# Performance work log

Hardware: AMD Instinct MI355X
Metric: run time of the kernel (lower is better)

The kernel has to match this reference:

```python
import math
import jax, jax.numpy as jnp
import numpy as np

N_HEAD = 16
N_EMBD = 1024
HEAD_DIM = N_EMBD // N_HEAD  # 64
GROUP_SIZE = 64
RESIDUAL_LEN = 32
K_BITS = 2
V_BITS = 2
CLIP = 10000.0


def _fake_quant(x, mn, mx, bits):
    # asymmetric min-max quantize-dequantize with straight-through estimator
    qmax = float(2 ** bits - 1)
    scale = jnp.maximum((mx - mn) / qmax, 1e-8)
    q = jnp.round((x - mn) / scale)
    deq = q * scale + mn
    return x + jax.lax.stop_gradient(deq - x)


def quantize_key(k):
    # per-channel over token groups: [B,H,S,D] -> groups of GROUP_SIZE tokens,
    # min/max over the token axis within each group, per head_dim channel
    B, H, S, D = k.shape
    k = jnp.clip(k, -CLIP, CLIP)
    kg = k.reshape(B, H, S // GROUP_SIZE, GROUP_SIZE, D)
    mn = kg.min(axis=3, keepdims=True)
    mx = kg.max(axis=3, keepdims=True)
    return _fake_quant(kg, mn, mx, K_BITS).reshape(B, H, S, D)


def quantize_value(v):
    # per-token over channel groups: groups of GROUP_SIZE along head_dim
    B, H, S, D = v.shape
    g = GROUP_SIZE if (GROUP_SIZE > 0 and D % GROUP_SIZE == 0) else D
    v = jnp.clip(v, -CLIP, CLIP)
    vg = v.reshape(B, H, S, D // g, g)
    mn = vg.min(axis=-1, keepdims=True)
    mx = vg.max(axis=-1, keepdims=True)
    return _fake_quant(vg, mn, mx, V_BITS).reshape(B, H, S, D)


def setup_inputs() -> dict:
    key = jax.random.key(0)
    ks = jax.random.split(key, 5)
    B, S = 2, 2048
    scale_in = 1.0 / math.sqrt(N_EMBD)
    return {
        "x": jax.random.normal(ks[0], (B, S, N_EMBD), jnp.float32),
        "W_qkv": jax.random.normal(ks[1], (N_EMBD, 3 * N_EMBD), jnp.float32) * scale_in,
        "b_qkv": jax.random.normal(ks[2], (3 * N_EMBD,), jnp.float32) * 0.01,
        "W_proj": jax.random.normal(ks[3], (N_EMBD, N_EMBD), jnp.float32) * scale_in,
        "b_proj": jax.random.normal(ks[4], (N_EMBD,), jnp.float32) * 0.01,
    }


def reference(x, W_qkv, b_qkv, W_proj, b_proj):
    B, S, E = x.shape
    H, D = N_HEAD, HEAD_DIM
    qkv = x @ W_qkv + b_qkv                       # [B,S,3E]
    q, k, v = jnp.split(qkv, 3, axis=-1)
    split = lambda t: t.reshape(B, S, H, D).transpose(0, 2, 1, 3)  # [B,H,S,D]
    q, k, v = split(q), split(k), split(v)

    # KIVI: quantize all keys up to multiple of RESIDUAL_LEN, values except last RESIDUAL_LEN tokens
    if S > RESIDUAL_LEN:
        kql = (S // RESIDUAL_LEN) * RESIDUAL_LEN
        if kql > 0:
            k = jnp.concatenate([quantize_key(k[:, :, :kql]), k[:, :, kql:]], axis=2)
        vql = max(0, S - RESIDUAL_LEN)
        if vql > 0:
            v = jnp.concatenate([quantize_value(v[:, :, :vql]), v[:, :, vql:]], axis=2)

    attn = jnp.einsum("bhqd,bhkd->bhqk", q, k) / math.sqrt(D)
    if S > 1:
        mask = jnp.tril(jnp.ones((S, S), bool))
        attn = jnp.where(mask[None, None], attn, -jnp.inf)
    att = jax.nn.softmax(attn, axis=-1)
    y = jnp.einsum("bhqk,bhkd->bhqd", att, v)     # [B,H,S,D]
    y = y.transpose(0, 2, 1, 3).reshape(B, S, E)
    return y @ W_proj + b_proj
```

## Files before the change

kernel.cpp:

```cpp
#include <hip/hip_runtime.h>
#include <math.h>

#define BATCH 2
#define SEQ   2048
#define NHEAD 16
#define EMB   1024
#define N3E   3072
#define VQL   2016
#define REC_CAP 65536

typedef unsigned short ushort8_t __attribute__((ext_vector_type(8)));
typedef unsigned short ushort4_t __attribute__((ext_vector_type(4)));
typedef short bf16x8 __attribute__((ext_vector_type(8)));
typedef float f32x4 __attribute__((ext_vector_type(4)));
typedef unsigned int uint2_t __attribute__((ext_vector_type(2)));

struct __align__(16) Rec { unsigned dst; unsigned mn_pack; float mn; float scale; };

__device__ __forceinline__ float clipf(float x) {
    return fminf(fmaxf(x, -10000.0f), 10000.0f);
}
__device__ __forceinline__ float bf2f(unsigned short u) {
    return __uint_as_float(((unsigned)u) << 16);
}
__device__ __forceinline__ unsigned short f2bf(float f) {
    unsigned u = __float_as_uint(f);
    unsigned r = 0x7FFFu + ((u >> 16) & 1u);
    return (unsigned short)((u + r) >> 16);
}
__device__ __forceinline__ unsigned cvtpk(float lo, float hi) {
    unsigned r;
    asm("v_cvt_pk_bf16_f32 %0, %1, %2" : "=v"(r) : "v"(lo), "v"(hi));
    return r;
}
__device__ __forceinline__ void async_copy16(const unsigned short* g, unsigned short* lds) {
    __builtin_amdgcn_global_load_lds(
        (const __attribute__((address_space(1))) unsigned int*)g,
        (__attribute__((address_space(3))) unsigned int*)lds, 16, 0, 0);
}

__global__ __launch_bounds__(256) void split_x_kernel(
    const float* __restrict__ X,
    unsigned short* __restrict__ Xh, unsigned short* __restrict__ Xm,
    unsigned* __restrict__ cnt)
{
    if (blockIdx.x == 0 && threadIdx.x == 0) *cnt = 0;
    const size_t i8 = ((size_t)blockIdx.x * 256 + threadIdx.x) * 8;
    float4 a = *(const float4*)(X + i8);
    float4 b = *(const float4*)(X + i8 + 4);
    float xs[8] = {a.x, a.y, a.z, a.w, b.x, b.y, b.z, b.w};
    ushort8_t h8, m8;
    #pragma unroll
    for (int j = 0; j < 8; ++j) {
        unsigned short h = f2bf(xs[j]);
        h8[j] = h;
        m8[j] = f2bf(xs[j] - bf2f(h));
    }
    *(ushort8_t*)(Xh + i8) = h8;
    *(ushort8_t*)(Xm + i8) = m8;
}

__global__ __launch_bounds__(256) void split_wt_kernel(
    const float* __restrict__ W,
    unsigned short* __restrict__ WTh, unsigned short* __restrict__ WTm,
    unsigned short* __restrict__ WTl)
{
    __shared__ float t[64][65];
    const int tid = threadIdx.x;
    const int nt = blockIdx.x * 64, kt = blockIdx.y * 64;
    const int r = tid >> 2, cg = (tid & 3) * 16;
    #pragma unroll
    for (int j = 0; j < 4; ++j) {
        float4 v = *(const float4*)(W + (size_t)(kt + r) * N3E + nt + cg + j * 4);
        t[r][cg + j * 4 + 0] = v.x; t[r][cg + j * 4 + 1] = v.y;
        t[r][cg + j * 4 + 2] = v.z; t[r][cg + j * 4 + 3] = v.w;
    }
    __syncthreads();
    ushort8_t h8[2], m8[2], l8[2];
    #pragma unroll
    for (int j = 0; j < 16; ++j) {
        float v = t[cg + j][r];
        unsigned short h = f2bf(v);
        float r1 = v - bf2f(h);
        unsigned short mm = f2bf(r1);
        float r2 = r1 - bf2f(mm);
        h8[j >> 3][j & 7] = h; m8[j >> 3][j & 7] = mm; l8[j >> 3][j & 7] = f2bf(r2);
    }
    size_t off = (size_t)(nt + r) * 1024 + kt + cg;
    *(ushort8_t*)(WTh + off) = h8[0]; *(ushort8_t*)(WTh + off + 8) = h8[1];
    *(ushort8_t*)(WTm + off) = m8[0]; *(ushort8_t*)(WTm + off + 8) = m8[1];
    *(ushort8_t*)(WTl + off) = l8[0]; *(ushort8_t*)(WTl + off + 8) = l8[1];
}

__device__ __forceinline__ void push_flag(unsigned* cnt, Rec* recs, unsigned dst,
                                          int mg, int ng, float mn, float scale) {
    unsigned idx = atomicAdd(cnt, 1u);
    if (idx < REC_CAP) {
        Rec r; r.dst = dst; r.mn_pack = (unsigned)mg | ((unsigned)ng << 12);
        r.mn = mn; r.scale = scale;
        recs[idx] = r;
    }
}

__global__ __launch_bounds__(256, 2) void gemm_qkv3(
    const unsigned short* __restrict__ Xh, const unsigned short* __restrict__ Xm,
    const unsigned short* __restrict__ WTh, const unsigned short* __restrict__ WTm,
    const float* __restrict__ bias,
    unsigned short* __restrict__ Qb, unsigned short* __restrict__ Kb,
    unsigned short* __restrict__ Vt,
    unsigned* __restrict__ cnt, Rec* __restrict__ recs)
{
    __shared__ __align__(16) unsigned short LDS[2][4][128 * 32];

    const int tid  = threadIdx.x;
    const int wave = tid >> 6, lane = tid & 63, lr = lane & 15, g = lane >> 4;
    const int wr = wave >> 1, wc = wave & 1;
    const int row0 = blockIdx.y * 128, col0 = blockIdx.x * 128;

    const int drow = lane >> 2;
    const int sgr  = ((lane & 3) ^ ((lane >> 3) & 3)) * 8;
    const unsigned short* tsrc =
        (wave == 0) ? Xh  + (size_t)(row0 + drow) * 1024 + sgr :
        (wave == 1) ? Xm  + (size_t)(row0 + drow) * 1024 + sgr :
        (wave == 2) ? WTh + (size_t)(col0 + drow) * 1024 + sgr :
                      WTm + (size_t)(col0 + drow) * 1024 + sgr;

    #define STAGE(buf, t)                                                        \
        _Pragma("unroll")                                                        \
        for (int c = 0; c < 8; ++c)                                              \
            async_copy16(tsrc + (size_t)(c * 16) * 1024 + (t) * 32,              \
                         &LDS[buf][wave][c * 16 * 32]);

    f32x4 acc[4][4] = {};

    const int rgr = (g ^ ((lr >> 1) & 3)) * 8;

    STAGE(0, 0);
    STAGE(1, 1);

    for (int t = 0; t < 32; ++t) {
        const int cur = t & 1;
        if (t < 31) {
            asm volatile("s_waitcnt vmcnt(8)" ::: "memory");
        } else {
            asm volatile("s_waitcnt vmcnt(0)" ::: "memory");
        }
        __builtin_amdgcn_s_barrier();

        bf16x8 axh[4], axm[4], bwh[4], bwm[4];
        #pragma unroll
        for (int mf = 0; mf < 4; ++mf) {
            axh[mf] = *(const bf16x8*)&LDS[cur][0][(wr * 64 + mf * 16 + lr) * 32 + rgr];
            axm[mf] = *(const bf16x8*)&LDS[cur][1][(wr * 64 + mf * 16 + lr) * 32 + rgr];
        }
        #pragma unroll
        for (int nf = 0; nf < 4; ++nf) {
            bwh[nf] = *(const bf16x8*)&LDS[cur][2][(wc * 64 + nf * 16 + lr) * 32 + rgr];
            bwm[nf] = *(const bf16x8*)&LDS[cur][3][(wc * 64 + nf * 16 + lr) * 32 + rgr];
        }
        asm volatile("s_waitcnt lgkmcnt(0)" ::: "memory");
        __builtin_amdgcn_sched_barrier(0);
        __builtin_amdgcn_s_barrier();

        if (t < 30) { STAGE(cur, t + 2); }

        #pragma unroll
        for (int nf = 0; nf < 4; ++nf) {
            #pragma unroll
            for (int mf = 0; mf < 4; ++mf)
                acc[mf][nf] = __builtin_amdgcn_mfma_f32_16x16x32_bf16(
                    axh[mf], bwh[nf], acc[mf][nf], 0, 0, 0);
            #pragma unroll
            for (int mf = 0; mf < 4; ++mf)
                acc[mf][nf] = __builtin_amdgcn_mfma_f32_16x16x32_bf16(
                    axh[mf], bwm[nf], acc[mf][nf], 0, 0, 0);
            #pragma unroll
            for (int mf = 0; mf < 4; ++mf)
                acc[mf][nf] = __builtin_amdgcn_mfma_f32_16x16x32_bf16(
                    axm[mf], bwh[nf], acc[mf][nf], 0, 0, 0);
        }
    }
    #undef STAGE

    const int which = col0 >> 10;
    const int hcol  = ((col0 + wc * 64) & 1023) >> 6;
    const int b     = row0 >> 11;
    const int s_base = (row0 & 2047) + wr * 64;

    float bo[4];
    #pragma unroll
    for (int n = 0; n < 4; ++n) bo[n] = bias[col0 + wc * 64 + n * 16 + lr];
    #pragma unroll
    for (int m = 0; m < 4; ++m)
        #pragma unroll
        for (int n = 0; n < 4; ++n)
            #pragma unroll
            for (int r = 0; r < 4; ++r)
                acc[m][n][r] += bo[n];

    if (which == 0) {
        unsigned short* qdst = Qb + (((size_t)b * NHEAD + hcol) * SEQ) * 64;
        #pragma unroll
        for (int m = 0; m < 4; ++m)
            #pragma unroll
            for (int r = 0; r < 4; ++r) {
                int s = s_base + m * 16 + g * 4 + r;
                #pragma unroll
                for (int n = 0; n < 4; ++n)
                    qdst[(size_t)s * 64 + n * 16 + lr] = f2bf(acc[m][n][r]);
            }
    } else if (which == 1) {
        #pragma unroll
        for (int n = 0; n < 4; ++n) {
            float cmn = INFINITY, cmx = -INFINITY;
            #pragma unroll
            for (int m = 0; m < 4; ++m)
                #pragma unroll
                for (int r = 0; r < 4; ++r) {
                    float v = clipf(acc[m][n][r]);
                    acc[m][n][r] = v;
                    cmn = fminf(cmn, v); cmx = fmaxf(cmx, v);
                }
            cmn = fminf(cmn, __shfl_xor(cmn, 16)); cmx = fmaxf(cmx, __shfl_xor(cmx, 16));
            cmn = fminf(cmn, __shfl_xor(cmn, 32)); cmx = fmaxf(cmx, __shfl_xor(cmx, 32));
            float scale = fmaxf((cmx - cmn) / 3.0f, 1e-8f);
            float tol = 0.5f - 1e-3f / scale;
            #pragma unroll
            for (int m = 0; m < 4; ++m)
                #pragma unroll
                for (int r = 0; r < 4; ++r) {
                    float f = (acc[m][n][r] - cmn) / scale;
                    float qv = rintf(f);
                    if (fabsf(f - qv) > tol) {
                        int s  = s_base + m * 16 + g * 4 + r;
                        int mg = row0 + wr * 64 + m * 16 + g * 4 + r;
                        int ng = col0 + wc * 64 + n * 16 + lr;
                        unsigned dst = 4194304u +
                            (unsigned)(((b * NHEAD + hcol) * SEQ + s) * 64 + n * 16 + lr);
                        push_flag(cnt, recs, dst, mg, ng, cmn, scale);
                    }
                    acc[m][n][r] = qv * scale + cmn;
                }
        }
        unsigned short* kdst = Kb + (((size_t)b * NHEAD + hcol) * SEQ) * 64;
        #pragma unroll
        for (int m = 0; m < 4; ++m)
            #pragma unroll
            for (int r = 0; r < 4; ++r) {
                int s = s_base + m * 16 + g * 4 + r;
                #pragma unroll
                for (int n = 0; n < 4; ++n)
                    kdst[(size_t)s * 64 + n * 16 + lr] = f2bf(acc[m][n][r]);
            }
    } else {
        #pragma unroll
        for (int m = 0; m < 4; ++m)
            #pragma unroll
            for (int r = 0; r < 4; ++r) {
                float c[4];
                #pragma unroll
                for (int n = 0; n < 4; ++n) c[n] = clipf(acc[m][n][r]);
                float mn = fminf(fminf(c[0], c[1]), fminf(c[2], c[3]));
                float mx = fmaxf(fmaxf(c[0], c[1]), fmaxf(c[2], c[3]));
                #pragma unroll
                for (int msk = 1; msk < 16; msk <<= 1) {
                    mn = fminf(mn, __shfl_xor(mn, msk));
                    mx = fmaxf(mx, __shfl_xor(mx, msk));
                }
                int s = s_base + m * 16 + g * 4 + r;
                if (s < VQL) {
                    float scale = fmaxf((mx - mn) / 3.0f, 1e-8f);
                    float tol = 0.5f - 1e-3f / scale;
                    #pragma unroll
                    for (int n = 0; n < 4; ++n) {
                        float f = (c[n] - mn) / scale;
                        float qv = rintf(f);
                        if (fabsf(f - qv) > tol) {
                            int mg = row0 + wr * 64 + m * 16 + g * 4 + r;
                            int ng = col0 + wc * 64 + n * 16 + lr;
                            unsigned dst = 8388608u +
                                (unsigned)((((b * NHEAD + hcol) * 64) + n * 16 + lr) * SEQ + s);
                            push_flag(cnt, recs, dst, mg, ng, mn, scale);
                        }
                        acc[m][n][r] = qv * scale + mn;
                    }
                }
            }
        #pragma unroll
        for (int m = 0; m < 4; ++m)
            #pragma unroll
            for (int n = 0; n < 4; ++n) {
                ushort4_t o;
                #pragma unroll
                for (int r = 0; r < 4; ++r) o[r] = f2bf(acc[m][n][r]);
                *(ushort4_t*)(Vt + ((((size_t)b * NHEAD + hcol) * 64) + n * 16 + lr) * SEQ
                                 + s_base + m * 16 + g * 4) = o;
            }
    }
}

__global__ __launch_bounds__(256) void repair_kernel(
    const float* __restrict__ X,
    const unsigned short* __restrict__ WTh, const unsigned short* __restrict__ WTm,
    const unsigned short* __restrict__ WTl,
    const float* __restrict__ bias, unsigned short* __restrict__ wsu,
    const unsigned* __restrict__ cnt, const Rec* __restrict__ recs)
{
    const int lane = threadIdx.x & 63;
    const int wid  = blockIdx.x * 4 + (threadIdx.x >> 6);
    unsigned nrec = *cnt; if (nrec > REC_CAP) nrec = REC_CAP;
    for (unsigned i = wid; i < nrec; i += gridDim.x * 4) {
        Rec rc = recs[i];
        int mg = rc.mn_pack & 4095;
        int ng = (rc.mn_pack >> 12) & 4095;
        const float* xr          = X   + (size_t)mg * 1024 + lane * 16;
        const unsigned short* wh = WTh + (size_t)ng * 1024 + lane * 16;
        const unsigned short* wm = WTm + (size_t)ng * 1024 + lane * 16;
        const unsigned short* wl = WTl + (size_t)ng * 1024 + lane * 16;
        float s = 0.f;
        #pragma unroll
        for (int j4 = 0; j4 < 4; ++j4) {
            float4 xv = *(const float4*)(xr + j4 * 4);
            float xs[4] = {xv.x, xv.y, xv.z, xv.w};
            #pragma unroll
            for (int e = 0; e < 4; ++e) {
                int j = j4 * 4 + e;
                s += xs[e] * (bf2f(wh[j]) + bf2f(wm[j]) + bf2f(wl[j]));
            }
        }
        #pragma unroll
        for (int msk = 1; msk < 64; msk <<= 1) s += __shfl_xor(s, msk);
        if (lane == 0) {
            float v = clipf(s + bias[ng]);
            float val = rintf((v - rc.mn) / rc.scale) * rc.scale + rc.mn;
            wsu[rc.dst] = f2bf(val);
        }
    }
}

__global__ __launch_bounds__(256) void attn_mfma(
    unsigned short* __restrict__ QY,
    const unsigned short* __restrict__ K,
    const unsigned short* __restrict__ Vt)
{
    __shared__ unsigned short Ks [64][72];
    __shared__ unsigned short VsT[64][72];
    __shared__ unsigned short Ps [4][16][72];

    const int tid  = threadIdx.x;
    const int wave = tid >> 6;
    const int lane = tid & 63;
    const int lr   = lane & 15;
    const int g    = lane >> 4;

    const int bid = blockIdx.x;
    const int qt  = 31 - (bid >> 5);
    const int bh  = bid & 31;
    const size_t base = (size_t)bh * (SEQ * 64);

    const int qrow = qt * 64 + wave * 16 + lr;
    const unsigned short* qp = QY + base + (size_t)qrow * 64;
    bf16x8 aq[2];
    #pragma unroll
    for (int ka = 0; ka < 2; ++ka)
        aq[ka] = *(const bf16x8*)(qp + ka * 32 + g * 8);

    f32x4 o[4] = {};
    float m[4]    = {-1e30f, -1e30f, -1e30f, -1e30f};
    float lsum[4] = {};
    const float sc = 0.125f;

    const int str = tid >> 2;
    const int stc = (tid & 3) << 4;

    for (int jt = 0; jt <= qt; ++jt) {
        __syncthreads();
        {
            const unsigned short* kg = K + base + ((size_t)(jt * 64 + str) << 6) + stc;
            *(ushort8_t*)&Ks[str][stc]     = *(const ushort8_t*)kg;
            *(ushort8_t*)&Ks[str][stc + 8] = *(const ushort8_t*)(kg + 8);
            const unsigned short* vg = Vt + base + ((size_t)str << 11) + jt * 64 + stc;
            *(ushort8_t*)&VsT[str][stc]     = *(const ushort8_t*)vg;
            *(ushort8_t*)&VsT[str][stc + 8] = *(const ushort8_t*)(vg + 8);
        }
        __syncthreads();

        f32x4 s[4] = {};
        #pragma unroll
        for (int f = 0; f < 4; ++f) {
            #pragma unroll
            for (int ka = 0; ka < 2; ++ka) {
                bf16x8 bk = *(const bf16x8*)&Ks[f * 16 + lr][ka * 32 + g * 8];
                s[f] = __builtin_amdgcn_mfma_f32_16x16x32_bf16(aq[ka], bk, s[f], 0, 0, 0);
            }
        }

        const bool diag = (jt == qt);
        float mx[4];
        #pragma unroll
        for (int r = 0; r < 4; ++r) {
            const int ql = wave * 16 + g * 4 + r;
            float vmax = -1e30f;
            #pragma unroll
            for (int f = 0; f < 4; ++f) {
                float v = s[f][r] * sc;
                if (diag && (f * 16 + lr) > ql) v = -1e30f;
                s[f][r] = v;
                vmax = fmaxf(vmax, v);
            }
            mx[r] = vmax;
        }
        #pragma unroll
        for (int msk = 1; msk < 16; msk <<= 1)
            #pragma unroll
            for (int r = 0; r < 4; ++r)
                mx[r] = fmaxf(mx[r], __shfl_xor(mx[r], msk));

        float alpha[4], tsum[4];
        #pragma unroll
        for (int r = 0; r < 4; ++r) {
            float mn = fmaxf(m[r], mx[r]);
            alpha[r] = __expf(m[r] - mn);
            m[r] = mn;
            float ts = 0.0f;
            #pragma unroll
            for (int f = 0; f < 4; ++f) {
                float p = __expf(s[f][r] - mn);
                unsigned short ub = f2bf(p);
                Ps[wave][g * 4 + r][f * 16 + lr] = ub;
                ts += bf2f(ub);
            }
            tsum[r] = ts;
        }
        #pragma unroll
        for (int msk = 1; msk < 16; msk <<= 1)
            #pragma unroll
            for (int r = 0; r < 4; ++r)
                tsum[r] += __shfl_xor(tsum[r], msk);
        #pragma unroll
        for (int r = 0; r < 4; ++r) {
            lsum[r] = lsum[r] * alpha[r] + tsum[r];
            #pragma unroll
            for (int df = 0; df < 4; ++df) o[df][r] *= alpha[r];
        }

        asm volatile("s_waitcnt lgkmcnt(0)" ::: "memory");
        __builtin_amdgcn_sched_barrier(0);

        bf16x8 pa[2];
        #pragma unroll
        for (int kb = 0; kb < 2; ++kb)
            pa[kb] = *(const bf16x8*)&Ps[wave][lr][kb * 32 + g * 8];
        #pragma unroll
        for (int df = 0; df < 4; ++df) {
            #pragma unroll
            for (int kb = 0; kb < 2; ++kb) {
                bf16x8 vb = *(const bf16x8*)&VsT[df * 16 + lr][kb * 32 + g * 8];
                o[df] = __builtin_amdgcn_mfma_f32_16x16x32_bf16(pa[kb], vb, o[df], 0, 0, 0);
            }
        }
    }

    float invl[4];
    #pragma unroll
    for (int r = 0; r < 4; ++r) invl[r] = 1.0f / lsum[r];
    #pragma unroll
    for (int df = 0; df < 4; ++df)
        #pragma unroll
        for (int r = 0; r < 4; ++r) {
            int q = qt * 64 + wave * 16 + g * 4 + r;
            QY[base + (size_t)q * 64 + df * 16 + lr] = f2bf(o[df][r] * invl[r]);
        }
}

#define PJ_PAD 72
__global__ __launch_bounds__(256, 2) void gemm_proj_mfma(
    const unsigned short* __restrict__ Y, const float* __restrict__ W,
    const float* __restrict__ bias, float* __restrict__ C)
{
    __shared__ unsigned short A2[2][128][PJ_PAD];
    __shared__ unsigned short B2[2][128][PJ_PAD];

    const int tid  = threadIdx.x;
    const int wave = tid >> 6, lane = tid & 63, lr = lane & 15, g = lane >> 4;
    const int wr = wave >> 1, wc = wave & 1;
    const int row0 = blockIdx.y * 128, col0 = blockIdx.x * 128;
    const int b = row0 >> 11, s0 = row0 & 2047;

    const int ra  = tid >> 1,       ca  = (tid & 1) * 32;
    const int cb4 = (tid & 31) * 4, kb4 = (tid >> 5) * 4;

    ushort8_t a_reg[4];
    float bw[2][4][4];

    {
        const unsigned short* gy = Y + ((((size_t)b * NHEAD + 0) * SEQ + s0 + ra) << 6) + ca;
        #pragma unroll
        for (int i = 0; i < 4; ++i) a_reg[i] = *(const ushort8_t*)(gy + i * 8);
        const float* gw = W + (size_t)kb4 * EMB + col0 + cb4;
        #pragma unroll
        for (int half = 0; half < 2; ++half)
            #pragma unroll
            for (int i = 0; i < 4; ++i)
                *(float4*)bw[half][i] = *(const float4*)(gw + (size_t)(half * 32 + i) * EMB);
        #pragma unroll
        for (int i = 0; i < 4; ++i) *(ushort8_t*)&A2[0][ra][ca + i * 8] = a_reg[i];
        #pragma unroll
        for (int half = 0; half < 2; ++half)
            #pragma unroll
            for (int j = 0; j < 4; ++j) {
                unsigned w2[2];
                w2[0] = cvtpk(bw[half][0][j], bw[half][1][j]);
                w2[1] = cvtpk(bw[half][2][j], bw[half][3][j]);
                *(uint2_t*)&B2[0][cb4 + j][half * 32 + kb4] = *(uint2_t*)w2;
            }
    }
    __syncthreads();

    f32x4 acc[4][4] = {};

    for (int t = 0; t < 16; ++t) {
        const int cur = t & 1;
        if (t < 15) {
            const unsigned short* gy =
                Y + ((((size_t)b * NHEAD + (t + 1)) * SEQ + s0 + ra) << 6) + ca;
            #pragma unroll
            for (int i = 0; i < 4; ++i) a_reg[i] = *(const ushort8_t*)(gy + i * 8);
            const float* gw = W + (size_t)((t + 1) * 64 + kb4) * EMB + col0 + cb4;
            #pragma unroll
            for (int half = 0; half < 2; ++half)
                #pragma unroll
                for (int i = 0; i < 4; ++i)
                    *(float4*)bw[half][i] = *(const float4*)(gw + (size_t)(half * 32 + i) * EMB);
        }
        #pragma unroll
        for (int kk = 0; kk < 2; ++kk) {
            bf16x8 af[4];
            #pragma unroll
            for (int m = 0; m < 4; ++m)
                af[m] = *(const bf16x8*)&A2[cur][wr * 64 + m * 16 + lr][kk * 32 + g * 8];
            #pragma unroll
            for (int n = 0; n < 4; ++n) {
                bf16x8 bf = *(const bf16x8*)&B2[cur][wc * 64 + n * 16 + lr][kk * 32 + g * 8];
                #pragma unroll
                for (int m = 0; m < 4; ++m)
                    acc[m][n] = __builtin_amdgcn_mfma_f32_16x16x32_bf16(af[m], bf, acc[m][n], 0, 0, 0);
            }
        }
        if (t < 15) {
            const int nxt = cur ^ 1;
            #pragma unroll
            for (int i = 0; i < 4; ++i) *(ushort8_t*)&A2[nxt][ra][ca + i * 8] = a_reg[i];
            #pragma unroll
            for (int half = 0; half < 2; ++half)
                #pragma unroll
                for (int j = 0; j < 4; ++j) {
                    unsigned w2[2];
                    w2[0] = cvtpk(bw[half][0][j], bw[half][1][j]);
                    w2[1] = cvtpk(bw[half][2][j], bw[half][3][j]);
                    *(uint2_t*)&B2[nxt][cb4 + j][half * 32 + kb4] = *(uint2_t*)w2;
                }
        }
        __syncthreads();
    }

    float bo[4];
    #pragma unroll
    for (int n = 0; n < 4; ++n) bo[n] = bias[col0 + wc * 64 + n * 16 + lr];
    #pragma unroll
    for (int m = 0; m < 4; ++m)
        #pragma unroll
        for (int r = 0; r < 4; ++r) {
            int mrow = row0 + wr * 64 + m * 16 + g * 4 + r;
            #pragma unroll
            for (int n = 0; n < 4; ++n)
                C[(size_t)mrow * EMB + col0 + wc * 64 + n * 16 + lr] = acc[m][n][r] + bo[n];
        }
}

extern "C" void kernel_launch(void* const* d_in, const int* in_sizes, int n_in,
                              void* d_out, int out_size, void* d_ws, size_t ws_size,
                              hipStream_t stream)
{
    const float* x     = (const float*)d_in[0];
    const float* Wqkv  = (const float*)d_in[1];
    const float* bqkv  = (const float*)d_in[2];
    const float* Wproj = (const float*)d_in[3];
    const float* bproj = (const float*)d_in[4];
    float* out = (float*)d_out;

    char* ws = (char*)d_ws;
    unsigned short* q   = (unsigned short*)ws;
    unsigned short* kb  = (unsigned short*)(ws + (8u  << 20));
    unsigned short* vt  = (unsigned short*)(ws + (16u << 20));
    unsigned short* Xh  = (unsigned short*)(ws + (24u << 20));
    unsigned short* Xm  = (unsigned short*)(ws + (32u << 20));
    unsigned short* WTh = (unsigned short*)(ws + (40u << 20));
    unsigned short* WTm = (unsigned short*)(ws + (46u << 20));
    unsigned short* WTl = (unsigned short*)(ws + (52u << 20));
    unsigned*       cnt = (unsigned*)(ws + (58u << 20));
    Rec*           recs = (Rec*)(ws + (58u << 20) + 256);

    split_x_kernel<<<2048, 256, 0, stream>>>(x, Xh, Xm, cnt);
    split_wt_kernel<<<dim3(48, 16), 256, 0, stream>>>(Wqkv, WTh, WTm, WTl);
    gemm_qkv3<<<dim3(N3E / 128, 4096 / 128), 256, 0, stream>>>(
        Xh, Xm, WTh, WTm, bqkv, q, kb, vt, cnt, recs);
    repair_kernel<<<128, 256, 0, stream>>>(x, WTh, WTm, WTl, bqkv,
                                           (unsigned short*)d_ws, cnt, recs);
    attn_mfma<<<dim3(32 * 32), 256, 0, stream>>>(q, kb, vt);
    gemm_proj_mfma<<<dim3(EMB / 128, 4096 / 128), 256, 0, stream>>>(q, Wproj, bproj, out);
}
```

Measured before the change: 321.9 us.

## Interleave LDS B-fragment loads with MFMA clusters in QKV GEMM loop

Splits the QKV GEMM inner loop so the B-fragment LDS reads for later column fragments are issued while MFMAs for earlier fragments run, with partial lgkmcnt waits instead of one full wait. Three of the four MFMA clusters run before the second barrier and the stage refill, and the last runs after the next async copy has been issued. s_setprio raises wave priority around the MFMA clusters. This is meant to hide LDS latency and overlap global prefetch with compute, but it depends on the manual wait counts being correct and may raise register pressure.

```diff
diff --git a/kernel.cpp b/kernel.cpp
--- a/kernel.cpp
+++ b/kernel.cpp
@@ -131,9 +131,25 @@
             async_copy16(tsrc + (size_t)(c * 16) * 1024 + (t) * 32,              \
                          &LDS[buf][wave][c * 16 * 32]);
 
+    #define CLUSTER(BH, BM, NF)                                                  \
+        _Pragma("unroll")                                                        \
+        for (int mf = 0; mf < 4; ++mf)                                           \
+            acc[mf][NF] = __builtin_amdgcn_mfma_f32_16x16x32_bf16(               \
+                axh[mf], BH, acc[mf][NF], 0, 0, 0);                              \
+        _Pragma("unroll")                                                        \
+        for (int mf = 0; mf < 4; ++mf)                                           \
+            acc[mf][NF] = __builtin_amdgcn_mfma_f32_16x16x32_bf16(               \
+                axh[mf], BM, acc[mf][NF], 0, 0, 0);                              \
+        _Pragma("unroll")                                                        \
+        for (int mf = 0; mf < 4; ++mf)                                           \
+            acc[mf][NF] = __builtin_amdgcn_mfma_f32_16x16x32_bf16(               \
+                axm[mf], BH, acc[mf][NF], 0, 0, 0);
+
     f32x4 acc[4][4] = {};
 
     const int rgr = (g ^ ((lr >> 1) & 3)) * 8;
+    const int arow = wr * 64 + lr;
+    const int brow = wc * 64 + lr;
 
     STAGE(0, 0);
     STAGE(1, 1);
@@ -147,40 +163,51 @@
         }
         __builtin_amdgcn_s_barrier();
 
-        bf16x8 axh[4], axm[4], bwh[4], bwm[4];
+        bf16x8 axh[4], axm[4];
         #pragma unroll
         for (int mf = 0; mf < 4; ++mf) {
-            axh[mf] = *(const bf16x8*)&LDS[cur][0][(wr * 64 + mf * 16 + lr) * 32 + rgr];
-            axm[mf] = *(const bf16x8*)&LDS[cur][1][(wr * 64 + mf * 16 + lr) * 32 + rgr];
-        }
-        #pragma unroll
-        for (int nf = 0; nf < 4; ++nf) {
-            bwh[nf] = *(const bf16x8*)&LDS[cur][2][(wc * 64 + nf * 16 + lr) * 32 + rgr];
-            bwm[nf] = *(const bf16x8*)&LDS[cur][3][(wc * 64 + nf * 16 + lr) * 32 + rgr];
-        }
+            axh[mf] = *(const bf16x8*)&LDS[cur][0][(arow + mf * 16) * 32 + rgr];
+            axm[mf] = *(const bf16x8*)&LDS[cur][1][(arow + mf * 16) * 32 + rgr];
+        }
+        bf16x8 bh0 = *(const bf16x8*)&LDS[cur][2][(brow +  0) * 32 + rgr];
+        bf16x8 bm0 = *(const bf16x8*)&LDS[cur][3][(brow +  0) * 32 + rgr];
+        bf16x8 bh1 = *(const bf16x8*)&LDS[cur][2][(brow + 16) * 32 + rgr];
+        bf16x8 bm1 = *(const bf16x8*)&LDS[cur][3][(brow + 16) * 32 + rgr];
+
+        asm volatile("s_waitcnt lgkmcnt(2)" ::: "memory");
+        __builtin_amdgcn_sched_barrier(0);
+        __builtin_amdgcn_s_setprio(1);
+        CLUSTER(bh0, bm0, 0)
+        __builtin_amdgcn_s_setprio(0);
+
+        bf16x8 bh2 = *(const bf16x8*)&LDS[cur][2][(brow + 32) * 32 + rgr];
+        bf16x8 bm2 = *(const bf16x8*)&LDS[cur][3][(brow + 32) * 32 + rgr];
+        asm volatile("s_waitcnt lgkmcnt(2)" ::: "memory");
+        __builtin_amdgcn_sched_barrier(0);
+        __builtin_amdgcn_s_setprio(1);
+        CLUSTER(bh1, bm1, 1)
+        __builtin_amdgcn_s_setprio(0);
+
+        bf16x8 bh3 = *(const bf16x8*)&LDS[cur][2][(brow + 48) * 32 + rgr];
+        bf16x8 bm3 = *(const bf16x8*)&LDS[cur][3][(brow + 48) * 32 + rgr];
+        asm volatile("s_waitcnt lgkmcnt(2)" ::: "memory");
+        __builtin_amdgcn_sched_barrier(0);
+        __builtin_amdgcn_s_setprio(1);
+        CLUSTER(bh2, bm2, 2)
+        __builtin_amdgcn_s_setprio(0);
+
         asm volatile("s_waitcnt lgkmcnt(0)" ::: "memory");
         __builtin_amdgcn_sched_barrier(0);
         __builtin_amdgcn_s_barrier();
 
         if (t < 30) { STAGE(cur, t + 2); }
 
-        #pragma unroll
-        for (int nf = 0; nf < 4; ++nf) {
-            #pragma unroll
-            for (int mf = 0; mf < 4; ++mf)
-                acc[mf][nf] = __builtin_amdgcn_mfma_f32_16x16x32_bf16(
-                    axh[mf], bwh[nf], acc[mf][nf], 0, 0, 0);
-            #pragma unroll
-            for (int mf = 0; mf < 4; ++mf)
-                acc[mf][nf] = __builtin_amdgcn_mfma_f32_16x16x32_bf16(
-                    axh[mf], bwm[nf], acc[mf][nf], 0, 0, 0);
-            #pragma unroll
-            for (int mf = 0; mf < 4; ++mf)
-                acc[mf][nf] = __builtin_amdgcn_mfma_f32_16x16x32_bf16(
-                    axm[mf], bwh[nf], acc[mf][nf], 0, 0, 0);
-        }
+        __builtin_amdgcn_s_setprio(1);
+        CLUSTER(bh3, bm3, 3)
+        __builtin_amdgcn_s_setprio(0);
     }
     #undef STAGE
+    #undef CLUSTER
 
     const int which = col0 >> 10;
     const int hcol  = ((col0 + wc * 64) & 1023) >> 6;
```

Result: no change. 325.9 us (+1.3%).

## Pre-tile and pre-swizzle split X and W operands into K-tile-major layout

Applied to the files above, without the earlier changes.

The split kernels now write the bf16 hi/mid parts of X and W^T in a K-tile-major layout: each 32-wide K slice is stored contiguously per row, with the XOR swizzle already applied. The QKV GEMM's async global-to-LDS copies then read fully contiguous 8KB chunks per stage instead of strided 64-byte row pieces. The repair kernel is updated to read the new layout. The aim is better coalescing of the staging loads, at the cost of strided reads in repair and different write patterns in the split kernels.

```diff
diff --git a/kernel.cpp b/kernel.cpp
--- a/kernel.cpp
+++ b/kernel.cpp
@@ -44,10 +44,13 @@
     unsigned short* __restrict__ Xh, unsigned short* __restrict__ Xm,
     unsigned* __restrict__ cnt)
 {
-    if (blockIdx.x == 0 && threadIdx.x == 0) *cnt = 0;
-    const size_t i8 = ((size_t)blockIdx.x * 256 + threadIdx.x) * 8;
-    float4 a = *(const float4*)(X + i8);
-    float4 b = *(const float4*)(X + i8 + 4);
+    if (blockIdx.x == 0 && blockIdx.y == 0 && threadIdx.x == 0) *cnt = 0;
+    const int t    = blockIdx.y;
+    const int row  = blockIdx.x * 64 + (threadIdx.x >> 2);
+    const int part = threadIdx.x & 3;
+    const float* src = X + (size_t)row * 1024 + t * 32 + part * 8;
+    float4 a = *(const float4*)src;
+    float4 b = *(const float4*)(src + 4);
     float xs[8] = {a.x, a.y, a.z, a.w, b.x, b.y, b.z, b.w};
     ushort8_t h8, m8;
     #pragma unroll
@@ -56,8 +59,10 @@
         h8[j] = h;
         m8[j] = f2bf(xs[j] - bf2f(h));
     }
-    *(ushort8_t*)(Xh + i8) = h8;
-    *(ushort8_t*)(Xm + i8) = m8;
+    const size_t base = ((size_t)t * 4096 + row) * 32;
+    const int pg = part ^ ((row >> 1) & 3);
+    *(ushort8_t*)(Xh + base + pg * 8) = h8;
+    *(ushort8_t*)(Xm + base + pg * 8) = m8;
 }
 
 __global__ __launch_bounds__(256) void split_wt_kernel(
@@ -86,10 +91,17 @@
         float r2 = r1 - bf2f(mm);
         h8[j >> 3][j & 7] = h; m8[j >> 3][j & 7] = mm; l8[j >> 3][j & 7] = f2bf(r2);
     }
-    size_t off = (size_t)(nt + r) * 1024 + kt + cg;
-    *(ushort8_t*)(WTh + off) = h8[0]; *(ushort8_t*)(WTh + off + 8) = h8[1];
-    *(ushort8_t*)(WTm + off) = m8[0]; *(ushort8_t*)(WTm + off + 8) = m8[1];
-    *(ushort8_t*)(WTl + off) = l8[0]; *(ushort8_t*)(WTl + off + 8) = l8[1];
+    const int col = nt + r;
+    const int t2  = (kt + cg) >> 5;
+    const int g0  = ((kt + cg) & 31) >> 3;
+    const int key = (col >> 1) & 3;
+    const size_t ob = ((size_t)t2 * 3072 + col) * 32;
+    *(ushort8_t*)(WTh + ob + ((g0 + 0) ^ key) * 8) = h8[0];
+    *(ushort8_t*)(WTh + ob + ((g0 + 1) ^ key) * 8) = h8[1];
+    *(ushort8_t*)(WTm + ob + ((g0 + 0) ^ key) * 8) = m8[0];
+    *(ushort8_t*)(WTm + ob + ((g0 + 1) ^ key) * 8) = m8[1];
+    size_t lo = (size_t)col * 1024 + kt + cg;
+    *(ushort8_t*)(WTl + lo) = l8[0]; *(ushort8_t*)(WTl + lo + 8) = l8[1];
 }
 
 __device__ __forceinline__ void push_flag(unsigned* cnt, Rec* recs, unsigned dst,
@@ -117,19 +129,17 @@
     const int wr = wave >> 1, wc = wave & 1;
     const int row0 = blockIdx.y * 128, col0 = blockIdx.x * 128;
 
-    const int drow = lane >> 2;
-    const int sgr  = ((lane & 3) ^ ((lane >> 3) & 3)) * 8;
-    const unsigned short* tsrc =
-        (wave == 0) ? Xh  + (size_t)(row0 + drow) * 1024 + sgr :
-        (wave == 1) ? Xm  + (size_t)(row0 + drow) * 1024 + sgr :
-        (wave == 2) ? WTh + (size_t)(col0 + drow) * 1024 + sgr :
-                      WTm + (size_t)(col0 + drow) * 1024 + sgr;
+    const unsigned short* tarr =
+        (wave == 0) ? Xh : (wave == 1) ? Xm : (wave == 2) ? WTh : WTm;
+    const int nr = (wave < 2) ? 4096 : 3072;
+    const unsigned short* tl =
+        tarr + (size_t)((wave < 2) ? row0 : col0) * 32 + lane * 8;
 
     #define STAGE(buf, t)                                                        \
         _Pragma("unroll")                                                        \
         for (int c = 0; c < 8; ++c)                                              \
-            async_copy16(tsrc + (size_t)(c * 16) * 1024 + (t) * 32,              \
-                         &LDS[buf][wave][c * 16 * 32]);
+            async_copy16(tl + ((size_t)(t) * nr) * 32 + c * 512,                 \
+                         &LDS[buf][wave][c * 512]);
 
     f32x4 acc[4][4] = {};
 
@@ -313,21 +323,26 @@
         Rec rc = recs[i];
         int mg = rc.mn_pack & 4095;
         int ng = (rc.mn_pack >> 12) & 4095;
-        const float* xr          = X   + (size_t)mg * 1024 + lane * 16;
-        const unsigned short* wh = WTh + (size_t)ng * 1024 + lane * 16;
-        const unsigned short* wm = WTm + (size_t)ng * 1024 + lane * 16;
-        const unsigned short* wl = WTl + (size_t)ng * 1024 + lane * 16;
+        const int t2  = lane >> 1;
+        const int g0  = (lane & 1) * 2;
+        const int key = (ng >> 1) & 3;
+        const size_t wb = ((size_t)t2 * 3072 + ng) * 32;
+        ushort8_t wh[2], wm[2], wl[2];
+        wh[0] = *(const ushort8_t*)(WTh + wb + ((g0 + 0) ^ key) * 8);
+        wh[1] = *(const ushort8_t*)(WTh + wb + ((g0 + 1) ^ key) * 8);
+        wm[0] = *(const ushort8_t*)(WTm + wb + ((g0 + 0) ^ key) * 8);
+        wm[1] = *(const ushort8_t*)(WTm + wb + ((g0 + 1) ^ key) * 8);
+        const unsigned short* wlp = WTl + (size_t)ng * 1024 + lane * 16;
+        wl[0] = *(const ushort8_t*)wlp;
+        wl[1] = *(const ushort8_t*)(wlp + 8);
+        const float* xr = X + (size_t)mg * 1024 + lane * 16;
         float s = 0.f;
         #pragma unroll
-        for (int j4 = 0; j4 < 4; ++j4) {
-            float4 xv = *(const float4*)(xr + j4 * 4);
-            float xs[4] = {xv.x, xv.y, xv.z, xv.w};
-            #pragma unroll
-            for (int e = 0; e < 4; ++e) {
-                int j = j4 * 4 + e;
-                s += xs[e] * (bf2f(wh[j]) + bf2f(wm[j]) + bf2f(wl[j]));
-            }
-        }
+        for (int gi = 0; gi < 2; ++gi)
+            #pragma unroll
+            for (int e = 0; e < 8; ++e)
+                s += xr[gi * 8 + e] *
+                     (bf2f(wh[gi][e]) + bf2f(wm[gi][e]) + bf2f(wl[gi][e]));
         #pragma unroll
         for (int msk = 1; msk < 64; msk <<= 1) s += __shfl_xor(s, msk);
         if (lane == 0) {
@@ -601,7 +616,7 @@
     unsigned*       cnt = (unsigned*)(ws + (58u << 20));
     Rec*           recs = (Rec*)(ws + (58u << 20) + 256);
 
-    split_x_kernel<<<2048, 256, 0, stream>>>(x, Xh, Xm, cnt);
+    split_x_kernel<<<dim3(64, 32), 256, 0, stream>>>(x, Xh, Xm, cnt);
     split_wt_kernel<<<dim3(48, 16), 256, 0, stream>>>(Wqkv, WTh, WTm, WTl);
     gemm_qkv3<<<dim3(N3E / 128, 4096 / 128), 256, 0, stream>>>(
         Xh, Xm, WTh, WTm, bqkv, q, kb, vt, cnt, recs);
```

Result: no change. 322.3 us (+0.1%).
